# Kernel tuning notes

Hardware: AMD Instinct MI355X
Metric: run time of the kernel (lower is better)

Reference implementation:

```python
import jax, jax.numpy as jnp
import numpy as np

B, H, KVH, D, CACHE = 16, 32, 8, 128, 4096


def _rope(x, cos, sin):
    # x: [B, S, Hx, D]; cos/sin: [B, S, 1, D//2] -- complex rotation on (even, odd) pairs
    xe, xo = x[..., ::2], x[..., 1::2]
    re = xe * cos - xo * sin
    im = xe * sin + xo * cos
    return jnp.stack([re, im], axis=-1).reshape(x.shape)


def setup_inputs() -> dict:
    key = jax.random.key(0)
    ks = jax.random.split(key, 8)
    xq = jax.random.normal(ks[0], (B, 1, H, D), jnp.float32)
    xk = jax.random.normal(ks[1], (B, 1, KVH, D), jnp.float32)
    xv = jax.random.normal(ks[2], (B, 1, KVH, D), jnp.float32)
    input_pos = jax.random.randint(ks[3], (B,), 1024, CACHE - 1, dtype=jnp.int32)
    inv_freq = 1.0 / (10000.0 ** (jnp.arange(0, D, 2, dtype=jnp.float32) / D))
    ang = input_pos.astype(jnp.float32)[:, None] * inv_freq[None, :]  # [B, D/2]
    freqs_cos = jnp.cos(ang)[:, None, :]  # [B, 1, D/2]
    freqs_sin = jnp.sin(ang)[:, None, :]
    cache_k = jax.random.randint(ks[4], (B, KVH, CACHE, D), -127, 128, dtype=jnp.int32)
    cache_v = jax.random.randint(ks[5], (B, KVH, CACHE, D), -127, 128, dtype=jnp.int32)
    k_scaler = jax.random.uniform(ks[6], (B, KVH, CACHE), jnp.float32, minval=0.005, maxval=0.05)
    v_scaler = jax.random.uniform(ks[7], (B, KVH, CACHE), jnp.float32, minval=0.005, maxval=0.05)
    return dict(xq=xq, xk=xk, xv=xv, freqs_cos=freqs_cos, freqs_sin=freqs_sin,
                k_scaler=k_scaler, v_scaler=v_scaler, cache_k=cache_k, cache_v=cache_v,
                input_pos=input_pos)


def reference(xq, xk, xv, freqs_cos, freqs_sin, k_scaler, v_scaler, cache_k, cache_v, input_pos):
    B_, S_, H_, D_ = xq.shape
    KVH_ = xk.shape[2]
    n_rep = H_ // KVH_
    cos, sin = freqs_cos[:, :, None, :], freqs_sin[:, :, None, :]
    q = _rope(xq, cos, sin)
    k = _rope(xk, cos, sin)
    # new decode token, [B, KVH, D]
    k_new = jnp.transpose(k, (0, 2, 1, 3))[:, :, 0, :]
    v_new = jnp.transpose(xv, (0, 2, 1, 3))[:, :, 0, :]
    # per-token, per-kv-head int8 quantization of the new K/V
    k_s = jnp.max(jnp.abs(k_new), axis=-1, keepdims=True) / 127.0 + 1e-8
    v_s = jnp.max(jnp.abs(v_new), axis=-1, keepdims=True) / 127.0 + 1e-8
    k_q = jnp.clip(jnp.round(k_new / k_s), -127, 127).astype(cache_k.dtype)
    v_q = jnp.clip(jnp.round(v_new / v_s), -127, 127).astype(cache_v.dtype)
    b_idx = jnp.arange(B_)
    cache_k = cache_k.at[b_idx, :, input_pos].set(k_q)
    cache_v = cache_v.at[b_idx, :, input_pos].set(v_q)
    k_scaler = k_scaler.at[b_idx, :, input_pos].set(k_s[..., 0])
    v_scaler = v_scaler.at[b_idx, :, input_pos].set(v_s[..., 0])
    # GQA: group query heads per kv head instead of materializing repeat_kv
    qg = jnp.transpose(q, (0, 2, 1, 3)).reshape(B_, KVH_, n_rep, D_)  # S_ == 1
    scores = jnp.einsum('bkrd,bksd->bkrs', qg, cache_k.astype(jnp.float32))
    scores = scores / jnp.sqrt(jnp.float32(D_)) * k_scaler[:, :, None, :]  # inline K dequant
    S_cache = cache_k.shape[2]
    mask = jnp.where(jnp.arange(S_cache)[None, :] <= input_pos[:, None], 0.0, -1e30)
    probs = jax.nn.softmax(scores + mask[:, None, None, :].astype(scores.dtype), axis=-1)
    out = jnp.einsum('bkrs,bksd->bkrd', probs * v_scaler[:, :, None, :], cache_v.astype(jnp.float32))
    return out.reshape(B_, H_, 1, D_)
```

## Files before the change

### kernel.cpp

```cpp
#include <hip/hip_runtime.h>
#include <hip/hip_bf16.h>
#include <cstdint>
#include <cstddef>

#define BATCH 16
#define HQ 32
#define KVHN 8
#define NREP 4
#define DIM 128
#define CACHE_LEN 4096
#define STATE_POS 128
#define NSTATE (CACHE_LEN / STATE_POS)

__global__ __launch_bounds__(64) void attn_partial(
    const float* __restrict__ xq,
    const float* __restrict__ fcos,
    const float* __restrict__ fsin,
    const float* __restrict__ k_scaler,
    const float* __restrict__ v_scaler,
    const int*   __restrict__ cache_k,
    const int*   __restrict__ cache_v,
    const int*   __restrict__ input_pos,
    float* __restrict__ ws_acc,
    float* __restrict__ ws_ml)
{
    const int state = blockIdx.x;
    const int kvh   = blockIdx.y;
    const int b     = blockIdx.z;
    const int pos   = input_pos[b];
    const int start = state * STATE_POS;
    if (start >= pos) return;

    const int lane = threadIdx.x;
    const int g    = lane >> 4;
    const int sl   = lane & 15;
    const int dA   = sl * 4;
    const int dB   = 64 + sl * 4;

    const int send = min(start + STATE_POS, pos);
    const float rsD = 0.088388347648318447f;

    float q[4][8];
    {
        float2 cA = *(const float2*)(fcos + b * 64 + 2 * sl);
        float2 sA = *(const float2*)(fsin + b * 64 + 2 * sl);
        float2 cB = *(const float2*)(fcos + b * 64 + 32 + 2 * sl);
        float2 sB = *(const float2*)(fsin + b * 64 + 32 + 2 * sl);
        cA.x *= rsD; cA.y *= rsD; cB.x *= rsD; cB.y *= rsD;
        sA.x *= rsD; sA.y *= rsD; sB.x *= rsD; sB.y *= rsD;
        #pragma unroll
        for (int r = 0; r < 4; ++r) {
            const float* qp = xq + ((size_t)(b * HQ + kvh * NREP + r)) * DIM;
            const float4 x0 = *(const float4*)(qp + dA);
            const float4 x1 = *(const float4*)(qp + dB);
            q[r][0] = x0.x * cA.x - x0.y * sA.x;
            q[r][1] = x0.x * sA.x + x0.y * cA.x;
            q[r][2] = x0.z * cA.y - x0.w * sA.y;
            q[r][3] = x0.z * sA.y + x0.w * cA.y;
            q[r][4] = x1.x * cB.x - x1.y * sB.x;
            q[r][5] = x1.x * sB.x + x1.y * cB.x;
            q[r][6] = x1.z * cB.y - x1.w * sB.y;
            q[r][7] = x1.z * sB.y + x1.w * cB.y;
        }
    }

    const int bk = b * KVHN + kvh;
    const int*   __restrict__ kb = cache_k + (size_t)bk * CACHE_LEN * DIM;
    const int*   __restrict__ vb = cache_v + (size_t)bk * CACHE_LEN * DIM;
    const float* __restrict__ ks = k_scaler + (size_t)bk * CACHE_LEN;
    const float* __restrict__ vs = v_scaler + (size_t)bk * CACHE_LEN;

    __shared__ float4 ssc4[STATE_POS];

    float mloc[4] = {-1e30f, -1e30f, -1e30f, -1e30f};

    #pragma unroll 4
    for (int i = 0; i < STATE_POS / 4; ++i) {
        const int s = start + i * 4 + g;
        const int* kp = kb + (size_t)s * DIM;
        const int4 kk0 = *(const int4*)(kp + dA);
        const int4 kk1 = *(const int4*)(kp + dB);
        const float k0 = (float)kk0.x, k1 = (float)kk0.y, k2 = (float)kk0.z, k3 = (float)kk0.w;
        const float k4 = (float)kk1.x, k5 = (float)kk1.y, k6 = (float)kk1.z, k7 = (float)kk1.w;
        float p[4];
        #pragma unroll
        for (int r = 0; r < 4; ++r) {
            p[r] = q[r][0] * k0 + q[r][1] * k1 + q[r][2] * k2 + q[r][3] * k3
                 + q[r][4] * k4 + q[r][5] * k5 + q[r][6] * k6 + q[r][7] * k7;
        }
        #pragma unroll
        for (int mask = 1; mask <= 8; mask <<= 1) {
            #pragma unroll
            for (int r = 0; r < 4; ++r) p[r] += __shfl_xor(p[r], mask, 64);
        }
        const float scale = ks[s];
        const bool valid = s < send;
        float4 sc;
        sc.x = valid ? p[0] * scale : -1e30f;
        sc.y = valid ? p[1] * scale : -1e30f;
        sc.z = valid ? p[2] * scale : -1e30f;
        sc.w = valid ? p[3] * scale : -1e30f;
        mloc[0] = fmaxf(mloc[0], sc.x);
        mloc[1] = fmaxf(mloc[1], sc.y);
        mloc[2] = fmaxf(mloc[2], sc.z);
        mloc[3] = fmaxf(mloc[3], sc.w);
        if (sl == 0) ssc4[i * 4 + g] = sc;
    }

    #pragma unroll
    for (int r = 0; r < 4; ++r) {
        mloc[r] = fmaxf(mloc[r], __shfl_xor(mloc[r], 16, 64));
        mloc[r] = fmaxf(mloc[r], __shfl_xor(mloc[r], 32, 64));
    }
    __syncthreads();

    float l[4] = {0.f, 0.f, 0.f, 0.f};
    float acc[4][8] = {};
    #pragma unroll 4
    for (int i = 0; i < STATE_POS / 4; ++i) {
        const int s = start + i * 4 + g;
        const int* vp = vb + (size_t)s * DIM;
        const int4 vv0 = *(const int4*)(vp + dA);
        const int4 vv1 = *(const int4*)(vp + dB);
        const float vsc = vs[s];
        const float4 sc = ssc4[i * 4 + g];
        const float v0 = (float)vv0.x, v1 = (float)vv0.y, v2 = (float)vv0.z, v3 = (float)vv0.w;
        const float v4 = (float)vv1.x, v5 = (float)vv1.y, v6 = (float)vv1.z, v7 = (float)vv1.w;
        const float scr[4] = {sc.x, sc.y, sc.z, sc.w};
        #pragma unroll
        for (int r = 0; r < 4; ++r) {
            const float pr = __expf(scr[r] - mloc[r]);
            l[r] += pr;
            const float pv = pr * vsc;
            acc[r][0] += pv * v0; acc[r][1] += pv * v1;
            acc[r][2] += pv * v2; acc[r][3] += pv * v3;
            acc[r][4] += pv * v4; acc[r][5] += pv * v5;
            acc[r][6] += pv * v6; acc[r][7] += pv * v7;
        }
    }

    #pragma unroll
    for (int mask = 16; mask <= 32; mask <<= 1) {
        #pragma unroll
        for (int r = 0; r < 4; ++r) {
            l[r] += __shfl_xor(l[r], mask, 64);
            #pragma unroll
            for (int c = 0; c < 8; ++c) acc[r][c] += __shfl_xor(acc[r][c], mask, 64);
        }
    }

    if (g == 0) {
        float* abase = ws_acc + (((size_t)bk * NSTATE + state) * 4) * DIM;
        #pragma unroll
        for (int r = 0; r < 4; ++r) {
            float4 a0 = make_float4(acc[r][0], acc[r][1], acc[r][2], acc[r][3]);
            float4 a1 = make_float4(acc[r][4], acc[r][5], acc[r][6], acc[r][7]);
            *(float4*)(abase + r * DIM + dA) = a0;
            *(float4*)(abase + r * DIM + dB) = a1;
        }
        if (sl == 0) {
            float* mlb = ws_ml + ((size_t)bk * NSTATE + state) * 8;
            #pragma unroll
            for (int r = 0; r < 4; ++r) { mlb[2 * r] = mloc[r]; mlb[2 * r + 1] = l[r]; }
        }
    }
}

__global__ __launch_bounds__(256) void attn_combine(
    const float* __restrict__ xq,
    const float* __restrict__ xk,
    const float* __restrict__ xv,
    const float* __restrict__ fcos,
    const float* __restrict__ fsin,
    const int*   __restrict__ input_pos,
    const float* __restrict__ ws_acc,
    const float* __restrict__ ws_ml,
    float* __restrict__ out)
{
    const int bk  = blockIdx.x;
    const int b   = bk >> 3;
    const int kvh = bk & 7;
    const int pos = input_pos[b];
    const int nst = min(NSTATE, (pos + STATE_POS - 1) / STATE_POS);

    const int t    = threadIdx.x;
    const int lane = t & 63;
    const int w    = t >> 6;

    __shared__ float sq[4][DIM];
    __shared__ float skq[DIM];
    __shared__ float svd[DIM];
    __shared__ float sml[NSTATE][8];
    __shared__ float ssc[4];
    __shared__ float sks, svs;

    const float rsD = 0.088388347648318447f;

    {
        const float c  = fcos[b * 64 + lane];
        const float s  = fsin[b * 64 + lane];
        const size_t qb = ((size_t)(b * HQ + kvh * NREP + w)) * DIM;
        const float xe = xq[qb + 2 * lane];
        const float xo = xq[qb + 2 * lane + 1];
        sq[w][2 * lane]     = xe * c - xo * s;
        sq[w][2 * lane + 1] = xe * s + xo * c;
    }
    if (w == 0) {
        const float c  = fcos[b * 64 + lane];
        const float s  = fsin[b * 64 + lane];
        const size_t kbb = ((size_t)(b * KVHN + kvh)) * DIM;
        const float xe = xk[kbb + 2 * lane];
        const float xo = xk[kbb + 2 * lane + 1];
        skq[2 * lane]     = xe * c - xo * s;
        skq[2 * lane + 1] = xe * s + xo * c;
    }
    for (int j = t; j < nst * 8; j += 256)
        sml[j >> 3][j & 7] = ws_ml[(size_t)bk * NSTATE * 8 + j];
    __syncthreads();

    if (w == 0) {
        float a = fmaxf(fabsf(skq[lane]), fabsf(skq[64 + lane]));
        #pragma unroll
        for (int mask = 32; mask; mask >>= 1) a = fmaxf(a, __shfl_xor(a, mask, 64));
        if (lane == 0) sks = a / 127.0f + 1e-8f;
    } else if (w == 1) {
        const size_t vbb = ((size_t)(b * KVHN + kvh)) * DIM;
        float a = fmaxf(fabsf(xv[vbb + lane]), fabsf(xv[vbb + 64 + lane]));
        #pragma unroll
        for (int mask = 32; mask; mask >>= 1) a = fmaxf(a, __shfl_xor(a, mask, 64));
        if (lane == 0) svs = a / 127.0f + 1e-8f;
    }
    __syncthreads();

    if (t < DIM) {
        skq[t] = fminf(fmaxf(rintf(skq[t] / sks), -127.f), 127.f);
    } else {
        const int d = t - DIM;
        const size_t vbb = ((size_t)(b * KVHN + kvh)) * DIM;
        const float vq = fminf(fmaxf(rintf(xv[vbb + d] / svs), -127.f), 127.f);
        svd[d] = vq * svs;
    }
    __syncthreads();

    {
        float sum = sq[w][lane] * skq[lane] + sq[w][64 + lane] * skq[64 + lane];
        #pragma unroll
        for (int mask = 32; mask; mask >>= 1) sum += __shfl_xor(sum, mask, 64);
        if (lane == 0) ssc[w] = sum * rsD * sks;
    }
    __syncthreads();

    const int r  = w;
    const int db = lane;
    float M = ssc[r];
    for (int s2 = 0; s2 < nst; ++s2) M = fmaxf(M, sml[s2][2 * r]);
    const float pn = __expf(ssc[r] - M);
    float L  = pn;
    float o0 = pn * svd[db];
    float o1 = pn * svd[db + 64];
    const float* ab = ws_acc + (size_t)bk * NSTATE * 4 * DIM;
    for (int s2 = 0; s2 < nst; ++s2) {
        const float al = __expf(sml[s2][2 * r] - M);
        L  += sml[s2][2 * r + 1] * al;
        o0 += ab[((size_t)(s2 * 4 + r)) * DIM + db]      * al;
        o1 += ab[((size_t)(s2 * 4 + r)) * DIM + db + 64] * al;
    }
    const float invL = 1.0f / L;
    float* ob = out + ((size_t)(b * HQ + kvh * NREP + r)) * DIM;
    ob[db]      = o0 * invL;
    ob[db + 64] = o1 * invL;
}

extern "C" void kernel_launch(void* const* d_in, const int* in_sizes, int n_in,
                              void* d_out, int out_size, void* d_ws, size_t ws_size,
                              hipStream_t stream)
{
    const float* xq        = (const float*)d_in[0];
    const float* xk        = (const float*)d_in[1];
    const float* xv        = (const float*)d_in[2];
    const float* fcos      = (const float*)d_in[3];
    const float* fsin      = (const float*)d_in[4];
    const float* k_scaler  = (const float*)d_in[5];
    const float* v_scaler  = (const float*)d_in[6];
    const int*   cache_k   = (const int*)d_in[7];
    const int*   cache_v   = (const int*)d_in[8];
    const int*   input_pos = (const int*)d_in[9];
    float* out = (float*)d_out;

    float* ws_acc = (float*)d_ws;
    float* ws_ml  = ws_acc + (size_t)BATCH * KVHN * NSTATE * 4 * DIM;

    dim3 g1(NSTATE, KVHN, BATCH);
    attn_partial<<<g1, 64, 0, stream>>>(xq, fcos, fsin, k_scaler, v_scaler,
                                        cache_k, cache_v, input_pos, ws_acc, ws_ml);
    attn_combine<<<BATCH * KVHN, 256, 0, stream>>>(xq, xk, xv, fcos, fsin,
                                                   input_pos, ws_acc, ws_ml, out);
}
```

Before: 503.2 us.

## Prefetch next K/V rows, stage scalers in LDS, transpose score reduction, rotate state order

Each loop iteration now loads the next K or V row into registers before computing on the current one (software double-buffering), and the per-position K and V scalers are staged into shared memory up front. The 4-head score reduction is restructured so that after two butterfly steps each lane picks one head and finishes the reduction with fewer shuffles. Lanes 0-3 each write one head's score and max. The block-to-state mapping is rotated by batch and head to spread skipped and active blocks more evenly across the grid. In exchange the kernel uses more registers and the mapping is harder to follow.

```diff
diff --git a/kernel.cpp b/kernel.cpp
--- a/kernel.cpp
+++ b/kernel.cpp
@@ -1,5 +1,4 @@
 #include <hip/hip_runtime.h>
-#include <hip/hip_bf16.h>
 #include <cstdint>
 #include <cstddef>
 
@@ -24,9 +23,9 @@
     float* __restrict__ ws_acc,
     float* __restrict__ ws_ml)
 {
-    const int state = blockIdx.x;
     const int kvh   = blockIdx.y;
     const int b     = blockIdx.z;
+    const int state = ((int)blockIdx.x + 5 * b + kvh) & (NSTATE - 1);
     const int pos   = input_pos[b];
     const int start = state * STATE_POS;
     if (start >= pos) return;
@@ -65,77 +64,103 @@
     }
 
     const int bk = b * KVHN + kvh;
-    const int*   __restrict__ kb = cache_k + (size_t)bk * CACHE_LEN * DIM;
-    const int*   __restrict__ vb = cache_v + (size_t)bk * CACHE_LEN * DIM;
-    const float* __restrict__ ks = k_scaler + (size_t)bk * CACHE_LEN;
-    const float* __restrict__ vs = v_scaler + (size_t)bk * CACHE_LEN;
+    const int*   __restrict__ kb  = cache_k + (size_t)bk * CACHE_LEN * DIM;
+    const int*   __restrict__ vbp = cache_v + (size_t)bk * CACHE_LEN * DIM;
+    const float* __restrict__ ks  = k_scaler + (size_t)bk * CACHE_LEN;
+    const float* __restrict__ vs  = v_scaler + (size_t)bk * CACHE_LEN;
 
     __shared__ float4 ssc4[STATE_POS];
-
-    float mloc[4] = {-1e30f, -1e30f, -1e30f, -1e30f};
-
-    #pragma unroll 4
-    for (int i = 0; i < STATE_POS / 4; ++i) {
-        const int s = start + i * 4 + g;
-        const int* kp = kb + (size_t)s * DIM;
-        const int4 kk0 = *(const int4*)(kp + dA);
-        const int4 kk1 = *(const int4*)(kp + dB);
-        const float k0 = (float)kk0.x, k1 = (float)kk0.y, k2 = (float)kk0.z, k3 = (float)kk0.w;
-        const float k4 = (float)kk1.x, k5 = (float)kk1.y, k6 = (float)kk1.z, k7 = (float)kk1.w;
-        float p[4];
-        #pragma unroll
-        for (int r = 0; r < 4; ++r) {
-            p[r] = q[r][0] * k0 + q[r][1] * k1 + q[r][2] * k2 + q[r][3] * k3
-                 + q[r][4] * k4 + q[r][5] * k5 + q[r][6] * k6 + q[r][7] * k7;
-        }
-        #pragma unroll
-        for (int mask = 1; mask <= 8; mask <<= 1) {
-            #pragma unroll
-            for (int r = 0; r < 4; ++r) p[r] += __shfl_xor(p[r], mask, 64);
-        }
-        const float scale = ks[s];
-        const bool valid = s < send;
-        float4 sc;
-        sc.x = valid ? p[0] * scale : -1e30f;
-        sc.y = valid ? p[1] * scale : -1e30f;
-        sc.z = valid ? p[2] * scale : -1e30f;
-        sc.w = valid ? p[3] * scale : -1e30f;
-        mloc[0] = fmaxf(mloc[0], sc.x);
-        mloc[1] = fmaxf(mloc[1], sc.y);
-        mloc[2] = fmaxf(mloc[2], sc.z);
-        mloc[3] = fmaxf(mloc[3], sc.w);
-        if (sl == 0) ssc4[i * 4 + g] = sc;
-    }
-
+    __shared__ float  sks_l[STATE_POS];
+    __shared__ float  svs_l[STATE_POS];
+
+    sks_l[lane]      = ks[start + lane];
+    sks_l[64 + lane] = ks[start + 64 + lane];
+    svs_l[lane]      = vs[start + lane];
+    svs_l[64 + lane] = vs[start + 64 + lane];
+
+    const bool h1  = (sl & 3) == 1;
+    const bool h2  = (sl & 3) == 2;
+    const bool h3  = (sl & 3) == 3;
+    const bool wlo = sl < 4;
+    const int  slast = start + 124 + g;
+
+    float mloc = -1e30f;
+
+    {
+        const int* kp0 = kb + (size_t)(start + g) * DIM;
+        int4 ka = *(const int4*)(kp0 + dA);
+        int4 kc = *(const int4*)(kp0 + dB);
+        #pragma unroll 4
+        for (int i = 0; i < STATE_POS / 4; ++i) {
+            const int s  = start + i * 4 + g;
+            const int sn = min(s + 4, slast);
+            const int* kpn = kb + (size_t)sn * DIM;
+            const int4 na = *(const int4*)(kpn + dA);
+            const int4 nc = *(const int4*)(kpn + dB);
+
+            const float k0 = (float)ka.x, k1 = (float)ka.y, k2 = (float)ka.z, k3 = (float)ka.w;
+            const float k4 = (float)kc.x, k5 = (float)kc.y, k6 = (float)kc.z, k7 = (float)kc.w;
+            float p[4];
+            #pragma unroll
+            for (int r = 0; r < 4; ++r) {
+                p[r] = q[r][0] * k0 + q[r][1] * k1 + q[r][2] * k2 + q[r][3] * k3
+                     + q[r][4] * k4 + q[r][5] * k5 + q[r][6] * k6 + q[r][7] * k7;
+            }
+            #pragma unroll
+            for (int r = 0; r < 4; ++r) {
+                p[r] += __shfl_xor(p[r], 1, 64);
+                p[r] += __shfl_xor(p[r], 2, 64);
+            }
+            float t = p[0];
+            t = h1 ? p[1] : t;
+            t = h2 ? p[2] : t;
+            t = h3 ? p[3] : t;
+            t += __shfl_xor(t, 4, 64);
+            t += __shfl_xor(t, 8, 64);
+            const float sc = (s < send) ? t * sks_l[i * 4 + g] : -1e30f;
+            mloc = fmaxf(mloc, sc);
+            if (wlo) ((float*)ssc4)[(i * 4 + g) * 4 + sl] = sc;
+            ka = na; kc = nc;
+        }
+    }
+
+    mloc = fmaxf(mloc, __shfl_xor(mloc, 16, 64));
+    mloc = fmaxf(mloc, __shfl_xor(mloc, 32, 64));
+    float mh[4];
     #pragma unroll
-    for (int r = 0; r < 4; ++r) {
-        mloc[r] = fmaxf(mloc[r], __shfl_xor(mloc[r], 16, 64));
-        mloc[r] = fmaxf(mloc[r], __shfl_xor(mloc[r], 32, 64));
-    }
+    for (int r = 0; r < 4; ++r) mh[r] = __shfl(mloc, r, 64);
     __syncthreads();
 
     float l[4] = {0.f, 0.f, 0.f, 0.f};
     float acc[4][8] = {};
-    #pragma unroll 4
-    for (int i = 0; i < STATE_POS / 4; ++i) {
-        const int s = start + i * 4 + g;
-        const int* vp = vb + (size_t)s * DIM;
-        const int4 vv0 = *(const int4*)(vp + dA);
-        const int4 vv1 = *(const int4*)(vp + dB);
-        const float vsc = vs[s];
-        const float4 sc = ssc4[i * 4 + g];
-        const float v0 = (float)vv0.x, v1 = (float)vv0.y, v2 = (float)vv0.z, v3 = (float)vv0.w;
-        const float v4 = (float)vv1.x, v5 = (float)vv1.y, v6 = (float)vv1.z, v7 = (float)vv1.w;
-        const float scr[4] = {sc.x, sc.y, sc.z, sc.w};
-        #pragma unroll
-        for (int r = 0; r < 4; ++r) {
-            const float pr = __expf(scr[r] - mloc[r]);
-            l[r] += pr;
-            const float pv = pr * vsc;
-            acc[r][0] += pv * v0; acc[r][1] += pv * v1;
-            acc[r][2] += pv * v2; acc[r][3] += pv * v3;
-            acc[r][4] += pv * v4; acc[r][5] += pv * v5;
-            acc[r][6] += pv * v6; acc[r][7] += pv * v7;
+    {
+        const int* vp0 = vbp + (size_t)(start + g) * DIM;
+        int4 va = *(const int4*)(vp0 + dA);
+        int4 vc = *(const int4*)(vp0 + dB);
+        #pragma unroll 4
+        for (int i = 0; i < STATE_POS / 4; ++i) {
+            const int s  = start + i * 4 + g;
+            const int sn = min(s + 4, slast);
+            const int* vpn = vbp + (size_t)sn * DIM;
+            const int4 na = *(const int4*)(vpn + dA);
+            const int4 nc = *(const int4*)(vpn + dB);
+
+            const float vsc = svs_l[i * 4 + g];
+            const float4 sc4 = ssc4[i * 4 + g];
+            const float v0 = (float)va.x, v1 = (float)va.y, v2 = (float)va.z, v3 = (float)va.w;
+            const float v4 = (float)vc.x, v5 = (float)vc.y, v6 = (float)vc.z, v7 = (float)vc.w;
+            const float scr[4] = {sc4.x, sc4.y, sc4.z, sc4.w};
+            #pragma unroll
+            for (int r = 0; r < 4; ++r) {
+                const float pr = __expf(scr[r] - mh[r]);
+                l[r] += pr;
+                const float pv = pr * vsc;
+                acc[r][0] += pv * v0; acc[r][1] += pv * v1;
+                acc[r][2] += pv * v2; acc[r][3] += pv * v3;
+                acc[r][4] += pv * v4; acc[r][5] += pv * v5;
+                acc[r][6] += pv * v6; acc[r][7] += pv * v7;
+            }
+            va = na; vc = nc;
         }
     }
 
@@ -161,7 +186,7 @@
         if (sl == 0) {
             float* mlb = ws_ml + ((size_t)bk * NSTATE + state) * 8;
             #pragma unroll
-            for (int r = 0; r < 4; ++r) { mlb[2 * r] = mloc[r]; mlb[2 * r + 1] = l[r]; }
+            for (int r = 0; r < 4; ++r) { mlb[2 * r] = mh[r]; mlb[2 * r + 1] = l[r]; }
         }
     }
 }
```

After: 502.5 us. No clear change (-0.1%).
